# Optimization experiments

Hardware: AMD Instinct MI355X
Metric: run time of the kernel (lower is better)

The kernel has to match this reference:

```python
import jax, jax.numpy as jnp
import numpy as np

N_NODES, F_IN, HID, HEADS, REP, NCLS = 8192, 128, 64, 8, 512, 32
E, NSYN, LMAX = 2048, 4096, 8
DM, DI, DSTATE, DCONV, DTR = 512, 1024, 16, 4, 32


def setup_inputs():
    key = jax.random.key(0)
    ks = jax.random.split(key, 24)
    g = lambda i, shape, s=0.05: jax.random.normal(ks[i], shape, jnp.float32) * s
    return {
        "edge_attr": jax.random.normal(ks[0], (E, 8), jnp.float32),
        "synapse": jax.random.normal(ks[1], (NSYN, 6), jnp.float32),
        "x_param": g(2, (N_NODES, F_IN), 0.1),
        "W1": g(3, (F_IN, HEADS * HID)),
        "att_src1": g(4, (HEADS, HID), 0.1),
        "att_dst1": g(5, (HEADS, HID), 0.1),
        "b1": jnp.zeros((HEADS * HID,), jnp.float32),
        "W2": g(6, (HEADS * HID, REP)),
        "att_src2": g(7, (1, REP), 0.1),
        "att_dst2": g(8, (1, REP), 0.1),
        "b2": jnp.zeros((REP,), jnp.float32),
        "W_in": g(9, (6, DM), 0.1),
        "b_in": jnp.zeros((DM,), jnp.float32),
        "W_inproj": g(10, (DM, 2 * DI)),
        "conv_w": g(11, (DI, DCONV), 0.1),
        "conv_b": jnp.zeros((DI,), jnp.float32),
        "W_xproj": g(12, (DI, DTR + 2 * DSTATE)),
        "W_dt": g(13, (DTR, DI), 0.1),
        "b_dt": jnp.full((DI,), -4.0, jnp.float32),
        "A_log": jnp.log(jnp.tile(jnp.arange(1, DSTATE + 1, dtype=jnp.float32), (DI, 1))),
        "D": jnp.ones((DI,), jnp.float32),
        "W_outproj": g(14, (DI, DM)),
        "W_lout": g(15, (DM, DM)),
        "b_lout": jnp.zeros((DM,), jnp.float32),
        "Wc1": g(16, (REP + 2 * DM, 512)),
        "bc1": jnp.zeros((512,), jnp.float32),
        "Wc2": g(17, (512, NCLS)),
        "bc2": jnp.zeros((NCLS,), jnp.float32),
        "edge_index": jax.random.randint(ks[18], (2, E), 0, N_NODES),
        "synapse_index": jnp.sort(jax.random.randint(ks[19], (NSYN,), 0, E)),
        "scatter_size": N_NODES,
    }


def _gat(x, W, a_src, a_dst, bias, src, dst, heads, out_ch, concat):
    # PyG GATConv (eval mode, edge_dim=None, self-loops already appended to src/dst)
    n = x.shape[0]
    xw = (x @ W).reshape(n, heads, out_ch)
    e = (xw * a_src).sum(-1)[src] + (xw * a_dst).sum(-1)[dst]  # [E+N, H]
    e = jax.nn.leaky_relu(e, 0.2)
    m = jax.ops.segment_max(e, dst, num_segments=n)
    ex = jnp.exp(e - m[dst])
    denom = jax.ops.segment_sum(ex, dst, num_segments=n)
    alpha = ex / denom[dst]
    out = jax.ops.segment_sum(alpha[:, :, None] * xw[src], dst, num_segments=n)
    out = out.reshape(n, heads * out_ch) if concat else out.mean(1)
    return out + bias


def _mamba_encoder(synapse, synapse_index, W_in, b_in, W_inproj, conv_w, conv_b,
                   W_xproj, W_dt, b_dt, A_log, D, W_outproj, W_lout, b_lout):
    # ragged [NSYN,6] -> padded [E, LMAX, 6] (synapse_index is sorted)
    counts = jax.ops.segment_sum(jnp.ones((NSYN,), jnp.int32), synapse_index, num_segments=E)
    starts = jnp.cumsum(counts) - counts
    pos = jnp.arange(NSYN) - starts[synapse_index]
    padded = jnp.zeros((E, LMAX, synapse.shape[1]), synapse.dtype).at[
        synapse_index, pos].set(synapse, mode="drop")
    u = padded @ W_in + b_in                     # linear_in: [E, L, DM]
    xz = u @ W_inproj                            # in_proj:   [E, L, 2*DI]
    xm, z = xz[..., :DI], xz[..., DI:]
    # depthwise causal conv over time
    xc = jax.lax.conv_general_dilated(
        xm.transpose(0, 2, 1), conv_w[:, None, :],
        window_strides=(1,), padding=[(DCONV - 1, 0)],
        dimension_numbers=("NCH", "OIH", "NCH"), feature_group_count=DI)
    xc = jax.nn.silu(xc + conv_b[:, None]).transpose(0, 2, 1)  # [E, L, DI]
    xdb = xc @ W_xproj
    dt = jax.nn.softplus(xdb[..., :DTR] @ W_dt + b_dt)         # [E, L, DI]
    Bm = xdb[..., DTR:DTR + DSTATE]                            # [E, L, N]
    Cm = xdb[..., DTR + DSTATE:]                               # [E, L, N]
    A = -jnp.exp(A_log)                                        # [DI, N]

    def step(h, t):
        dt_t, B_t, C_t, x_t = t                                # [E,DI],[E,N],[E,N],[E,DI]
        h = jnp.exp(dt_t[:, :, None] * A) * h + (dt_t * x_t)[:, :, None] * B_t[:, None, :]
        return h, jnp.einsum("bdn,bn->bd", h, C_t)

    h0 = jnp.zeros((E, DI, DSTATE), xc.dtype)
    _, ys = jax.lax.scan(step, h0, (dt.transpose(1, 0, 2), Bm.transpose(1, 0, 2),
                                    Cm.transpose(1, 0, 2), xc.transpose(1, 0, 2)))
    y = ys.transpose(1, 0, 2) + D * xc                         # [E, L, DI]
    out = (y * jax.nn.silu(z)) @ W_outproj                     # [E, L, DM]
    # masked mean over true sequence length (empty groups behave like a zero seq of len 1)
    cnt = jnp.clip(counts, 1, LMAX).astype(out.dtype)
    mask = (jnp.arange(LMAX)[None, :] < cnt[:, None]).astype(out.dtype)
    pooled = (out * mask[:, :, None]).sum(1) / cnt[:, None]
    return pooled @ W_lout + b_lout                            # [E, DM]


def _forward(edge_attr, synapse, x_param, W1, att_src1, att_dst1, b1,
             W2, att_src2, att_dst2, b2, W_in, b_in, W_inproj, conv_w, conv_b,
             W_xproj, W_dt, b_dt, A_log, D, W_outproj, W_lout, b_lout,
             Wc1, bc1, Wc2, bc2, edge_index, synapse_index, scatter_size):
    # GAT stack (eval: dropouts identity; edge_attr unused since edge_dim=None)
    loops = jnp.arange(N_NODES)
    src = jnp.concatenate([edge_index[0], loops])
    dst = jnp.concatenate([edge_index[1], loops])
    h = jax.nn.elu(_gat(x_param, W1, att_src1, att_dst1, b1, src, dst, HEADS, HID, True))
    h = _gat(h, W2, att_src2, att_dst2, b2, src, dst, 1, REP, False)   # [N, REP]
    x_point = _mamba_encoder(synapse, synapse_index, W_in, b_in, W_inproj, conv_w,
                             conv_b, W_xproj, W_dt, b_dt, A_log, D, W_outproj,
                             W_lout, b_lout)                            # [E, DM]

    def smax(idx):
        s = jax.ops.segment_max(x_point, idx, num_segments=scatter_size)
        nz = jax.ops.segment_sum(jnp.ones((E,), jnp.int32), idx, num_segments=scatter_size)
        return jnp.where(nz[:, None] > 0, s, 0.0)  # torch_scatter: empty slots -> 0

    left, right = smax(edge_index[0]), smax(edge_index[1])
    feats = jnp.concatenate([h, left, right], axis=1)          # [N, REP+2*DM]
    return jax.nn.relu(feats @ Wc1 + bc1) @ Wc2 + bc2          # [N, NCLS]


def reference(edge_attr, synapse, x_param, W1, att_src1, att_dst1, b1,
              W2, att_src2, att_dst2, b2, W_in, b_in, W_inproj, conv_w, conv_b,
              W_xproj, W_dt, b_dt, A_log, D, W_outproj, W_lout, b_lout,
              Wc1, bc1, Wc2, bc2, edge_index, synapse_index, scatter_size):
    return _forward(edge_attr, synapse, x_param, W1, att_src1, att_dst1, b1,
                    W2, att_src2, att_dst2, b2, W_in, b_in, W_inproj, conv_w, conv_b,
                    W_xproj, W_dt, b_dt, A_log, D, W_outproj, W_lout, b_lout,
                    Wc1, bc1, Wc2, bc2, edge_index, synapse_index, scatter_size)
```

## Files before the change

kernel.cpp:

```cpp
#include <hip/hip_runtime.h>

#define N_NODES 8192
#define F_IN 128
#define HID 64
#define HEADS 8
#define REP 512
#define NCLS 32
#define E_EDGES 2048
#define NSYN 4096
#define LMAX 8
#define DM 512
#define DI 1024
#define DSTATE 16
#define DCONV 4
#define DTR 32
#define TOT_EDGES (E_EDGES + N_NODES)
#define ROWS (E_EDGES * LMAX)
#define MC_CAP 6144

typedef short bf16x8 __attribute__((ext_vector_type(8)));
typedef float f32x4 __attribute__((ext_vector_type(4)));

__device__ __forceinline__ unsigned mapf(float f) {
  unsigned u = __float_as_uint(f);
  return (u & 0x80000000u) ? ~u : (u | 0x80000000u);
}
__device__ __forceinline__ float unmapf(unsigned u) {
  return __uint_as_float((u & 0x80000000u) ? (u ^ 0x80000000u) : ~u);
}
__device__ __forceinline__ float fsig(float x) {
  return __builtin_amdgcn_rcpf(1.0f + __expf(-x));
}
__device__ __forceinline__ float fsoftplus(float x) {
  return fmaxf(x, 0.0f) + __logf(1.0f + __expf(-fabsf(x)));
}
__device__ __forceinline__ unsigned short f2bf(float f) {
  unsigned u = __float_as_uint(f);
  unsigned r = (u + 0x7FFFu + ((u >> 16) & 1u)) >> 16;
  return (unsigned short)r;
}
__device__ __forceinline__ float bf2f(unsigned short h) {
  return __uint_as_float(((unsigned)h) << 16);
}
__device__ __forceinline__ void split2(float x, unsigned short* hh, unsigned short* ll) {
  unsigned short h = f2bf(x);
  *hh = h;
  *ll = f2bf(x - bf2f(h));
}
__device__ __forceinline__ int lower_bound_dev(const int* __restrict__ arr, int n, int v) {
  int lo = 0, hi = n;
  while (lo < hi) { int mid = (lo + hi) >> 1; if (arr[mid] < v) lo = mid + 1; else hi = mid; }
  return lo;
}
__device__ __forceinline__ int src_of(const int* __restrict__ ei, int i) {
  return i < E_EDGES ? ei[i] : i - E_EDGES;
}
__device__ __forceinline__ int dst_of(const int* __restrict__ ei, int i) {
  return i < E_EDGES ? ei[E_EDGES + i] : i - E_EDGES;
}
__device__ __forceinline__ int clip_cnt(int c) { return c < 1 ? 1 : (c > LMAX ? LMAX : c); }

__global__ __launch_bounds__(256) void gemm_mfma(
    const unsigned short* __restrict__ Ah, const unsigned short* __restrict__ Al,
    const unsigned short* __restrict__ Bth, const unsigned short* __restrict__ Btl,
    float* __restrict__ C, int M, int N, int K,
    const float* __restrict__ bias, int act) {
  __shared__ __align__(16) unsigned short As[2][64][40];
  const int tid = threadIdx.x;
  const int w = tid >> 6;
  const int lane = tid & 63;
  const int brow = blockIdx.y * 64;
  const int bcol = blockIdx.x * 64;
  const int srow = tid >> 2;
  const int skc = tid & 3;
  const int r0 = lane & 15;
  const int kg = lane >> 4;
  f32x4 acc[4] = {};
  const size_t aoff = (size_t)(brow + srow) * K + skc * 8;
  const size_t boff = (size_t)(bcol + w * 16 + r0) * K + kg * 8;
  bf16x8 bh = *(const bf16x8*)(Bth + boff);
  bf16x8 bl = *(const bf16x8*)(Btl + boff);
  *(bf16x8*)(&As[0][srow][skc * 8]) = *(const bf16x8*)(Ah + aoff);
  *(bf16x8*)(&As[1][srow][skc * 8]) = *(const bf16x8*)(Al + aoff);
  __syncthreads();
  for (int kt = 0; kt < K; kt += 32) {
    const bool more = (kt + 32) < K;
    bf16x8 nAh, nAl, nbh, nbl;
    if (more) {
      nAh = *(const bf16x8*)(Ah + aoff + kt + 32);
      nAl = *(const bf16x8*)(Al + aoff + kt + 32);
      nbh = *(const bf16x8*)(Bth + boff + kt + 32);
      nbl = *(const bf16x8*)(Btl + boff + kt + 32);
    }
#pragma unroll
    for (int r = 0; r < 4; ++r) {
      bf16x8 ah = *(const bf16x8*)(&As[0][r * 16 + r0][kg * 8]);
      bf16x8 al = *(const bf16x8*)(&As[1][r * 16 + r0][kg * 8]);
      acc[r] = __builtin_amdgcn_mfma_f32_16x16x32_bf16(ah, bh, acc[r], 0, 0, 0);
      acc[r] = __builtin_amdgcn_mfma_f32_16x16x32_bf16(ah, bl, acc[r], 0, 0, 0);
      acc[r] = __builtin_amdgcn_mfma_f32_16x16x32_bf16(al, bh, acc[r], 0, 0, 0);
    }
    __syncthreads();
    if (more) {
      *(bf16x8*)(&As[0][srow][skc * 8]) = nAh;
      *(bf16x8*)(&As[1][srow][skc * 8]) = nAl;
      bh = nbh; bl = nbl;
    }
    __syncthreads();
  }
  const int col = bcol + w * 16 + r0;
  const float bb = bias ? bias[col] : 0.0f;
#pragma unroll
  for (int r = 0; r < 4; ++r) {
#pragma unroll
    for (int j = 0; j < 4; ++j) {
      int row = brow + r * 16 + kg * 4 + j;
      float v = acc[r][j] + bb;
      if (act == 1) v = fmaxf(v, 0.0f);
      C[(size_t)row * N + col] = v;
    }
  }
}

__global__ __launch_bounds__(512) void gemm_mfma2(
    const unsigned short* __restrict__ Ah, const unsigned short* __restrict__ Al,
    const unsigned short* __restrict__ Bth, const unsigned short* __restrict__ Btl,
    float* __restrict__ C, int M, int N, int K,
    const float* __restrict__ bias, int act) {
  __shared__ __align__(16) unsigned short As[2][128][40];
  __shared__ __align__(16) unsigned short Bs[2][128][40];
  const int tid = threadIdx.x;
  const int w = tid >> 6;
  const int lane = tid & 63;
  const int wr = w >> 2, wc = w & 3;
  const int mb = M >> 7;
  const int lin = blockIdx.x;
  const int bx = lin / mb;
  const int by = lin % mb;
  const int brow = by * 128;
  const int bcol = bx * 128;
  const int r0 = lane & 15;
  const int kg = lane >> 4;
  const int row0 = tid >> 2, kc0 = tid & 3;
  const size_t a0 = (size_t)(brow + row0) * K + kc0 * 8;
  const size_t b0 = (size_t)(bcol + row0) * K + kc0 * 8;
  f32x4 acc[4][2] = {};
  {
    bf16x8 t0 = *(const bf16x8*)(Ah + a0), t1 = *(const bf16x8*)(Al + a0);
    bf16x8 t2 = *(const bf16x8*)(Bth + b0), t3 = *(const bf16x8*)(Btl + b0);
    *(bf16x8*)(&As[0][row0][kc0 * 8]) = t0;
    *(bf16x8*)(&As[1][row0][kc0 * 8]) = t1;
    *(bf16x8*)(&Bs[0][row0][kc0 * 8]) = t2;
    *(bf16x8*)(&Bs[1][row0][kc0 * 8]) = t3;
  }
  __syncthreads();
  for (int kt = 0; kt < K; kt += 32) {
    const bool more = (kt + 32) < K;
    bf16x8 p0, p1, p2, p3;
    if (more) {
      p0 = *(const bf16x8*)(Ah + a0 + kt + 32);
      p1 = *(const bf16x8*)(Al + a0 + kt + 32);
      p2 = *(const bf16x8*)(Bth + b0 + kt + 32);
      p3 = *(const bf16x8*)(Btl + b0 + kt + 32);
    }
    bf16x8 bhv[2], blv[2];
#pragma unroll
    for (int cf = 0; cf < 2; ++cf) {
      bhv[cf] = *(const bf16x8*)(&Bs[0][wc * 32 + cf * 16 + r0][kg * 8]);
      blv[cf] = *(const bf16x8*)(&Bs[1][wc * 32 + cf * 16 + r0][kg * 8]);
    }
#pragma unroll
    for (int rf = 0; rf < 4; ++rf) {
      bf16x8 ah = *(const bf16x8*)(&As[0][wr * 64 + rf * 16 + r0][kg * 8]);
      bf16x8 al = *(const bf16x8*)(&As[1][wr * 64 + rf * 16 + r0][kg * 8]);
#pragma unroll
      for (int cf = 0; cf < 2; ++cf) {
        acc[rf][cf] = __builtin_amdgcn_mfma_f32_16x16x32_bf16(ah, bhv[cf], acc[rf][cf], 0, 0, 0);
        acc[rf][cf] = __builtin_amdgcn_mfma_f32_16x16x32_bf16(ah, blv[cf], acc[rf][cf], 0, 0, 0);
        acc[rf][cf] = __builtin_amdgcn_mfma_f32_16x16x32_bf16(al, bhv[cf], acc[rf][cf], 0, 0, 0);
      }
    }
    __syncthreads();
    if (more) {
      *(bf16x8*)(&As[0][row0][kc0 * 8]) = p0;
      *(bf16x8*)(&As[1][row0][kc0 * 8]) = p1;
      *(bf16x8*)(&Bs[0][row0][kc0 * 8]) = p2;
      *(bf16x8*)(&Bs[1][row0][kc0 * 8]) = p3;
    }
    __syncthreads();
  }
#pragma unroll
  for (int rf = 0; rf < 4; ++rf)
#pragma unroll
    for (int cf = 0; cf < 2; ++cf) {
      int col = bcol + wc * 32 + cf * 16 + r0;
      float bb = bias ? bias[col] : 0.0f;
#pragma unroll
      for (int j = 0; j < 4; ++j) {
        int row = brow + wr * 64 + rf * 16 + kg * 4 + j;
        float v = acc[rf][cf][j] + bb;
        if (act == 1) v = fmaxf(v, 0.0f);
        C[(size_t)row * N + col] = v;
      }
    }
}

__global__ __launch_bounds__(256) void gemm_mfma_sk(
    const unsigned short* __restrict__ Ah, const unsigned short* __restrict__ Al,
    const unsigned short* __restrict__ Bth, const unsigned short* __restrict__ Btl,
    float* __restrict__ C, int M, int N, int K) {
  __shared__ __align__(16) unsigned short As[2][64][40];
  const int tid = threadIdx.x;
  const int w = tid >> 6;
  const int lane = tid & 63;
  const int brow = blockIdx.y * 64;
  const int bcol = blockIdx.x * 64;
  const int srow = tid >> 2;
  const int skc = tid & 3;
  const int r0 = lane & 15;
  const int kg = lane >> 4;
  const int kchunk = K / gridDim.z;
  const int k0 = blockIdx.z * kchunk;
  f32x4 acc[4] = {};
  const size_t aoff = (size_t)(brow + srow) * K;
  const size_t boff = (size_t)(bcol + w * 16 + r0) * K + kg * 8;
  for (int kt = k0; kt < k0 + kchunk; kt += 32) {
    bf16x8 bh = *(const bf16x8*)(Bth + boff + kt);
    bf16x8 bl = *(const bf16x8*)(Btl + boff + kt);
    *(bf16x8*)(&As[0][srow][skc * 8]) = *(const bf16x8*)(Ah + aoff + kt + skc * 8);
    *(bf16x8*)(&As[1][srow][skc * 8]) = *(const bf16x8*)(Al + aoff + kt + skc * 8);
    __syncthreads();
#pragma unroll
    for (int r = 0; r < 4; ++r) {
      bf16x8 ah = *(const bf16x8*)(&As[0][r * 16 + r0][kg * 8]);
      bf16x8 al = *(const bf16x8*)(&As[1][r * 16 + r0][kg * 8]);
      acc[r] = __builtin_amdgcn_mfma_f32_16x16x32_bf16(ah, bh, acc[r], 0, 0, 0);
      acc[r] = __builtin_amdgcn_mfma_f32_16x16x32_bf16(ah, bl, acc[r], 0, 0, 0);
      acc[r] = __builtin_amdgcn_mfma_f32_16x16x32_bf16(al, bh, acc[r], 0, 0, 0);
    }
    __syncthreads();
  }
  const int col = bcol + w * 16 + r0;
#pragma unroll
  for (int r = 0; r < 4; ++r) {
#pragma unroll
    for (int j = 0; j < 4; ++j) {
      int row = brow + r * 16 + kg * 4 + j;
      atomicAdd(&C[(size_t)row * N + col], acc[r][j]);
    }
  }
}

__global__ void split_kernel(const float* __restrict__ x, unsigned short* __restrict__ h,
                             unsigned short* __restrict__ l, int n) {
  int i = blockIdx.x * 256 + threadIdx.x;
  if (i >= n) return;
  split2(x[i], &h[i], &l[i]);
}

__global__ void tsplit_kernel(const float* __restrict__ W, unsigned short* __restrict__ Wth,
                              unsigned short* __restrict__ Wtl, int K, int N) {
  int i = blockIdx.x * 256 + threadIdx.x;
  if (i >= K * N) return;
  int k = i / N, n = i - k * N;
  float v = W[i];
  unsigned short h = f2bf(v);
  Wth[(size_t)n * K + k] = h;
  Wtl[(size_t)n * K + k] = f2bf(v - bf2f(h));
}

template <int BM, int BN>
__global__ __launch_bounds__(256) void gemm_t(
    const float* __restrict__ A, int lda,
    const float* __restrict__ B, int ldb,
    float* __restrict__ C, int ldc,
    int M, int N, int K,
    const float* __restrict__ bias, int act) {
  constexpr int RR = BM / 64;
  constexpr int CR = BN / 64;
  __shared__ float As[16][BM + 4];
  __shared__ float Bs[16][BN + 4];
  const int tid = threadIdx.x;
  const int tx = tid & 15;
  const int ty = tid >> 4;
  const int brow = blockIdx.y * BM;
  const int bcol = blockIdx.x * BN;
  float acc[RR][CR][4][4] = {};
  for (int kt = 0; kt < K; kt += 16) {
#pragma unroll
    for (int p = 0; p < RR; ++p) {
      int c = tid + p * 256;
      int row = c >> 2, kc = c & 3;
      int gr = brow + row;
      float4 v = make_float4(0.f, 0.f, 0.f, 0.f);
      if (gr < M) v = *reinterpret_cast<const float4*>(A + (size_t)gr * lda + kt + kc * 4);
      As[kc * 4 + 0][row] = v.x;
      As[kc * 4 + 1][row] = v.y;
      As[kc * 4 + 2][row] = v.z;
      As[kc * 4 + 3][row] = v.w;
    }
#pragma unroll
    for (int p = 0; p < CR; ++p) {
      int c = tid + p * 256;
      int k = c / (BN / 4), c4 = c % (BN / 4);
      int gc = bcol + c4 * 4;
      float4 v = make_float4(0.f, 0.f, 0.f, 0.f);
      if (gc < N) v = *reinterpret_cast<const float4*>(B + (size_t)(kt + k) * ldb + gc);
      *reinterpret_cast<float4*>(&Bs[k][c4 * 4]) = v;
    }
    __syncthreads();
#pragma unroll
    for (int k = 0; k < 16; ++k) {
      float av[RR * 4], bv[CR * 4];
#pragma unroll
      for (int r = 0; r < RR; ++r) {
        float4 t = *reinterpret_cast<const float4*>(&As[k][r * 64 + ty * 4]);
        av[r * 4 + 0] = t.x; av[r * 4 + 1] = t.y; av[r * 4 + 2] = t.z; av[r * 4 + 3] = t.w;
      }
#pragma unroll
      for (int cq = 0; cq < CR; ++cq) {
        float4 t = *reinterpret_cast<const float4*>(&Bs[k][cq * 64 + tx * 4]);
        bv[cq * 4 + 0] = t.x; bv[cq * 4 + 1] = t.y; bv[cq * 4 + 2] = t.z; bv[cq * 4 + 3] = t.w;
      }
#pragma unroll
      for (int r = 0; r < RR; ++r)
#pragma unroll
        for (int cq = 0; cq < CR; ++cq)
#pragma unroll
          for (int i = 0; i < 4; ++i)
#pragma unroll
            for (int j = 0; j < 4; ++j)
              acc[r][cq][i][j] = fmaf(av[r * 4 + i], bv[cq * 4 + j], acc[r][cq][i][j]);
    }
    __syncthreads();
  }
#pragma unroll
  for (int r = 0; r < RR; ++r)
#pragma unroll
    for (int i = 0; i < 4; ++i) {
      int row = brow + r * 64 + ty * 4 + i;
      if (row >= M) continue;
#pragma unroll
      for (int cq = 0; cq < CR; ++cq) {
        int col = bcol + cq * 64 + tx * 4;
        if (col >= N) continue;
        float4 v;
        v.x = acc[r][cq][i][0]; v.y = acc[r][cq][i][1];
        v.z = acc[r][cq][i][2]; v.w = acc[r][cq][i][3];
        if (bias) {
          float4 bb = *reinterpret_cast<const float4*>(bias + col);
          v.x += bb.x; v.y += bb.y; v.z += bb.z; v.w += bb.w;
        }
        if (act == 1) {
          v.x = fmaxf(v.x, 0.f); v.y = fmaxf(v.y, 0.f);
          v.z = fmaxf(v.z, 0.f); v.w = fmaxf(v.w, 0.f);
        }
        *reinterpret_cast<float4*>(C + (size_t)row * ldc + col) = v;
      }
    }
}

__global__ void counts_kernel(const int* __restrict__ sidx, int* __restrict__ counts) {
  int e = blockIdx.x * 256 + threadIdx.x;
  if (e >= E_EDGES) return;
  int lo = lower_bound_dev(sidx, NSYN, e);
  int hi = lower_bound_dev(sidx, NSYN, e + 1);
  counts[e] = hi - lo;
}

__global__ void scatter_padded_kernel(const float* __restrict__ synapse,
                                      const int* __restrict__ sidx,
                                      float* __restrict__ padded) {
  int i = blockIdx.x * 256 + threadIdx.x;
  if (i >= NSYN) return;
  int e = sidx[i];
  int lo = lower_bound_dev(sidx, NSYN, e);
  int pos = i - lo;
  if (pos < LMAX) {
#pragma unroll
    for (int c = 0; c < 6; ++c) padded[((size_t)e * LMAX + pos) * 6 + c] = synapse[(size_t)i * 6 + c];
  }
}

__global__ __launch_bounds__(256) void prefix_kernel(const int* __restrict__ counts,
                                                     int* __restrict__ starts_c) {
  __shared__ int part[256];
  int t = threadIdx.x;
  int loc[8];
  int s = 0;
#pragma unroll
  for (int i = 0; i < 8; ++i) {
    int c = clip_cnt(counts[t * 8 + i]);
    loc[i] = s;
    s += c;
  }
  part[t] = s;
  __syncthreads();
  int mytot = s;
  for (int o = 1; o < 256; o <<= 1) {
    int add = (t >= o) ? part[t - o] : 0;
    __syncthreads();
    part[t] += add;
    __syncthreads();
  }
  int off = part[t] - mytot;
#pragma unroll
  for (int i = 0; i < 8; ++i) starts_c[t * 8 + i] = off + loc[i];
}

__global__ __launch_bounds__(256) void xc_compact_kernel(
    const float* __restrict__ padded,
    const float* __restrict__ W_eff, const float* __restrict__ b_eff,
    const float* __restrict__ conv_w, const float* __restrict__ conv_b,
    const int* __restrict__ counts, const int* __restrict__ starts_c,
    unsigned short* __restrict__ xch, unsigned short* __restrict__ xcl) {
  __shared__ float pads[LMAX * 6];
  int t = threadIdx.x;
  int d = blockIdx.x * 256 + t;
  int e = blockIdx.y;
  if (t < LMAX * 6) pads[t] = padded[(size_t)e * LMAX * 6 + t];
  __syncthreads();
  int cnt = clip_cnt(counts[e]);
  int sc = starts_c[e];
  float wef[6];
#pragma unroll
  for (int c = 0; c < 6; ++c) wef[c] = W_eff[c * 2048 + d];
  float cw0 = conv_w[d * 4 + 0], cw1 = conv_w[d * 4 + 1];
  float cw2 = conv_w[d * 4 + 2], cw3 = conv_w[d * 4 + 3];
  float cb = conv_b[d], be = b_eff[d];
  float x0 = 0.f, x1 = 0.f, x2 = 0.f;
  for (int l = 0; l < cnt; ++l) {
    float xm = be;
#pragma unroll
    for (int c = 0; c < 6; ++c) xm += pads[l * 6 + c] * wef[c];
    float s0 = cb + xm * cw3;
    if (l >= 1) s0 += x2 * cw2;
    if (l >= 2) s0 += x1 * cw1;
    if (l >= 3) s0 += x0 * cw0;
    float v = s0 * fsig(s0);
    size_t o = (size_t)(sc + l) * DI + d;
    split2(v, &xch[o], &xcl[o]);
    x0 = x1; x1 = x2; x2 = xm;
  }
}

__global__ __launch_bounds__(256) void mamba_scan_pool_kernel(
    const float* __restrict__ xdb_c, const float* __restrict__ padded,
    const float* __restrict__ W_eff, const float* __restrict__ b_eff,
    const float* __restrict__ W_dt, const float* __restrict__ b_dt,
    const float* __restrict__ A_log, const float* __restrict__ Dv,
    const float* __restrict__ conv_w, const float* __restrict__ conv_b,
    const int* __restrict__ counts, const int* __restrict__ starts_c,
    unsigned short* __restrict__ pooledh, unsigned short* __restrict__ pooledl) {
  __shared__ float pads[LMAX * 6];
  int t = threadIdx.x;
  int d = blockIdx.x * 256 + t;
  int e = blockIdx.y;
  if (t < LMAX * 6) pads[t] = padded[(size_t)e * LMAX * 6 + t];
  float wdt[DTR];
#pragma unroll
  for (int k = 0; k < DTR; ++k) wdt[k] = W_dt[k * DI + d];
  float a[DSTATE];
#pragma unroll
  for (int n = 0; n < DSTATE; ++n) a[n] = -__expf(A_log[d * DSTATE + n]);
  float h[DSTATE];
#pragma unroll
  for (int n = 0; n < DSTATE; ++n) h[n] = 0.0f;
  float wef[6], wez[6];
#pragma unroll
  for (int c = 0; c < 6; ++c) {
    wef[c] = W_eff[c * 2048 + d];
    wez[c] = W_eff[c * 2048 + DI + d];
  }
  float cw0 = conv_w[d * 4 + 0], cw1 = conv_w[d * 4 + 1];
  float cw2 = conv_w[d * 4 + 2], cw3 = conv_w[d * 4 + 3];
  float cb = conv_b[d];
  float bdt = b_dt[d], Dd = Dv[d], be = b_eff[d], bez = b_eff[DI + d];
  __syncthreads();
  int cnt = clip_cnt(counts[e]);
  int sc = starts_c[e];
  float x0 = 0.f, x1 = 0.f, x2 = 0.f;
  float ssum = 0.0f;
  for (int l = 0; l < cnt; ++l) {
    float xm = be;
#pragma unroll
    for (int c = 0; c < 6; ++c) xm += pads[l * 6 + c] * wef[c];
    float s0 = cb + xm * cw3;
    if (l >= 1) s0 += x2 * cw2;
    if (l >= 2) s0 += x1 * cw1;
    if (l >= 3) s0 += x0 * cw0;
    float xt = s0 * fsig(s0);
    const float* __restrict__ xrow = xdb_c + (size_t)(sc + l) * 64;
    float acc = bdt;
#pragma unroll
    for (int k = 0; k < DTR; ++k) acc += xrow[k] * wdt[k];
    float dt = fsoftplus(acc);
    float dtx = dt * xt;
    float y = 0.0f;
#pragma unroll
    for (int n = 0; n < DSTATE; ++n) {
      float en = __expf(dt * a[n]);
      h[n] = en * h[n] + dtx * xrow[32 + n];
      y += h[n] * xrow[48 + n];
    }
    y += Dd * xt;
    float z = bez;
#pragma unroll
    for (int c = 0; c < 6; ++c) z += pads[l * 6 + c] * wez[c];
    ssum += y * z * fsig(z);
    x0 = x1; x1 = x2; x2 = xm;
  }
  float pv = ssum / (float)cnt;
  split2(pv, &pooledh[(size_t)e * DI + d], &pooledl[(size_t)e * DI + d]);
}

__global__ void esed1_kernel(const float* __restrict__ xw1, const float* __restrict__ as1,
                             const float* __restrict__ ad1, float* __restrict__ es1,
                             float* __restrict__ ed1) {
  int idx = blockIdx.x * 256 + threadIdx.x;
  int n = idx >> 3, h = idx & 7;
  const float* xr = xw1 + (size_t)n * 512 + h * 64;
  const float* sr = as1 + h * 64;
  const float* dr = ad1 + h * 64;
  float es = 0.0f, ed = 0.0f;
#pragma unroll
  for (int c = 0; c < 64; ++c) { float v = xr[c]; es += v * sr[c]; ed += v * dr[c]; }
  es1[idx] = es; ed1[idx] = ed;
}

__global__ void edge1_kernel(const int* __restrict__ ei, const float* __restrict__ es1,
                             const float* __restrict__ ed1, float* __restrict__ e1,
                             unsigned* __restrict__ m1u) {
  int idx = blockIdx.x * 256 + threadIdx.x;
  if (idx >= TOT_EDGES * HEADS) return;
  int i = idx >> 3, h = idx & 7;
  int s = src_of(ei, i), d = dst_of(ei, i);
  float v = es1[s * 8 + h] + ed1[d * 8 + h];
  v = v >= 0.0f ? v : 0.2f * v;
  e1[idx] = v;
  atomicMax(m1u + d * 8 + h, mapf(v));
}

__global__ void ex1_kernel(const int* __restrict__ ei, float* __restrict__ e1,
                           const unsigned* __restrict__ m1u, float* __restrict__ denom1) {
  int idx = blockIdx.x * 256 + threadIdx.x;
  if (idx >= TOT_EDGES * HEADS) return;
  int i = idx >> 3, h = idx & 7;
  int d = dst_of(ei, i);
  float ex = expf(e1[idx] - unmapf(m1u[d * 8 + h]));
  e1[idx] = ex;
  atomicAdd(denom1 + d * 8 + h, ex);
}

__global__ void selfinit1_kernel(const float* __restrict__ e1, const float* __restrict__ denom1,
                                 const float* __restrict__ xw1, float* __restrict__ g1) {
  int idx = blockIdx.x * 256 + threadIdx.x;
  int n = idx >> 9, j = idx & 511;
  int h = j >> 6;
  float alpha = e1[(size_t)(E_EDGES + n) * 8 + h] / denom1[n * 8 + h];
  g1[idx] = alpha * xw1[idx];
}

__global__ __launch_bounds__(256) void agg1_kernel(const int* __restrict__ ei,
                                                   const float* __restrict__ e1,
                                                   const float* __restrict__ denom1,
                                                   const float* __restrict__ xw1,
                                                   float* __restrict__ g1) {
  int i = blockIdx.x;
  int s = ei[i], d = ei[E_EDGES + i];
  for (int j = threadIdx.x; j < 512; j += 256) {
    int h = j >> 6;
    float alpha = e1[i * 8 + h] / denom1[d * 8 + h];
    atomicAdd(g1 + (size_t)d * 512 + j, alpha * xw1[(size_t)s * 512 + j]);
  }
}

__global__ void elu_bias_split_kernel(const float* __restrict__ g1, const float* __restrict__ b1,
                                      unsigned short* __restrict__ g1h,
                                      unsigned short* __restrict__ g1l) {
  int idx = blockIdx.x * 256 + threadIdx.x;
  int j = idx & 511;
  float v = g1[idx] + b1[j];
  v = v > 0.0f ? v : expm1f(v);
  split2(v, &g1h[idx], &g1l[idx]);
}

__global__ __launch_bounds__(64) void esed2_kernel(const float* __restrict__ xw2,
                                                   const float* __restrict__ as2,
                                                   const float* __restrict__ ad2,
                                                   float* __restrict__ es2,
                                                   float* __restrict__ ed2) {
  int n = blockIdx.x, t = threadIdx.x;
  float es = 0.0f, ed = 0.0f;
  for (int c = t; c < 512; c += 64) {
    float v = xw2[(size_t)n * 512 + c];
    es += v * as2[c]; ed += v * ad2[c];
  }
#pragma unroll
  for (int o = 32; o > 0; o >>= 1) { es += __shfl_down(es, o, 64); ed += __shfl_down(ed, o, 64); }
  if (t == 0) { es2[n] = es; ed2[n] = ed; }
}

__global__ void edge2_kernel(const int* __restrict__ ei, const float* __restrict__ es2,
                             const float* __restrict__ ed2, float* __restrict__ e2,
                             unsigned* __restrict__ m2u) {
  int i = blockIdx.x * 256 + threadIdx.x;
  if (i >= TOT_EDGES) return;
  int s = src_of(ei, i), d = dst_of(ei, i);
  float v = es2[s] + ed2[d];
  v = v >= 0.0f ? v : 0.2f * v;
  e2[i] = v;
  atomicMax(m2u + d, mapf(v));
}

__global__ void ex2_kernel(const int* __restrict__ ei, float* __restrict__ e2,
                           const unsigned* __restrict__ m2u, float* __restrict__ denom2) {
  int i = blockIdx.x * 256 + threadIdx.x;
  if (i >= TOT_EDGES) return;
  int d = dst_of(ei, i);
  float ex = expf(e2[i] - unmapf(m2u[d]));
  e2[i] = ex;
  atomicAdd(denom2 + d, ex);
}

__global__ void selfinit2_kernel(const float* __restrict__ e2, const float* __restrict__ denom2,
                                 const float* __restrict__ xw2, float* __restrict__ g2) {
  int idx = blockIdx.x * 256 + threadIdx.x;
  int n = idx >> 9;
  float alpha = e2[E_EDGES + n] / denom2[n];
  g2[idx] = alpha * xw2[idx];
}

__global__ __launch_bounds__(256) void agg2_kernel(const int* __restrict__ ei,
                                                   const float* __restrict__ e2,
                                                   const float* __restrict__ denom2,
                                                   const float* __restrict__ xw2,
                                                   float* __restrict__ g2) {
  int i = blockIdx.x;
  int s = ei[i], d = ei[E_EDGES + i];
  float alpha = e2[i] / denom2[d];
  for (int j = threadIdx.x; j < 512; j += 256) {
    atomicAdd(g2 + (size_t)d * 512 + j, alpha * xw2[(size_t)s * 512 + j]);
  }
}

__global__ __launch_bounds__(256) void leftright_kernel(const int* __restrict__ ei,
                                                        const float* __restrict__ xp,
                                                        unsigned* __restrict__ leftU,
                                                        unsigned* __restrict__ rightU,
                                                        int* __restrict__ flagL,
                                                        int* __restrict__ flagR) {
  int i = blockIdx.x;
  int s = ei[i], d = ei[E_EDGES + i];
  if (threadIdx.x == 0) { flagL[s] = 1; flagR[d] = 1; }
  for (int j = threadIdx.x; j < 512; j += 256) {
    unsigned v = mapf(xp[(size_t)i * 512 + j]);
    atomicMax(leftU + (size_t)s * 512 + j, v);
    atomicMax(rightU + (size_t)d * 512 + j, v);
  }
}

__global__ void concat_split_kernel(const float* __restrict__ g2, const float* __restrict__ b2,
                                    const unsigned* __restrict__ leftU,
                                    const unsigned* __restrict__ rightU,
                                    const int* __restrict__ flagL, const int* __restrict__ flagR,
                                    unsigned short* __restrict__ fh,
                                    unsigned short* __restrict__ fl) {
  int idx = blockIdx.x * 256 + threadIdx.x;
  int n = idx >> 9, j = idx & 511;
  size_t base = (size_t)n * 1536 + j;
  split2(g2[idx] + b2[j], &fh[base], &fl[base]);
  split2(flagL[n] ? unmapf(leftU[idx]) : 0.0f, &fh[base + 512], &fl[base + 512]);
  split2(flagR[n] ? unmapf(rightU[idx]) : 0.0f, &fh[base + 1024], &fl[base + 1024]);
}

extern "C" void kernel_launch(void* const* d_in, const int* in_sizes, int n_in,
                              void* d_out, int out_size, void* d_ws, size_t ws_size,
                              hipStream_t stream) {
  const float* synapse = (const float*)d_in[1];
  const float* x_param = (const float*)d_in[2];
  const float* W1 = (const float*)d_in[3];
  const float* as1 = (const float*)d_in[4];
  const float* ad1 = (const float*)d_in[5];
  const float* b1 = (const float*)d_in[6];
  const float* W2 = (const float*)d_in[7];
  const float* as2 = (const float*)d_in[8];
  const float* ad2 = (const float*)d_in[9];
  const float* b2 = (const float*)d_in[10];
  const float* W_in = (const float*)d_in[11];
  const float* b_in = (const float*)d_in[12];
  const float* W_inproj = (const float*)d_in[13];
  const float* conv_w = (const float*)d_in[14];
  const float* conv_b = (const float*)d_in[15];
  const float* W_xproj = (const float*)d_in[16];
  const float* W_dt = (const float*)d_in[17];
  const float* b_dt = (const float*)d_in[18];
  const float* A_log = (const float*)d_in[19];
  const float* Dv = (const float*)d_in[20];
  const float* W_outproj = (const float*)d_in[21];
  const float* W_lout = (const float*)d_in[22];
  const float* b_lout = (const float*)d_in[23];
  const float* Wc1 = (const float*)d_in[24];
  const float* bc1 = (const float*)d_in[25];
  const float* Wc2 = (const float*)d_in[26];
  const float* bc2 = (const float*)d_in[27];
  const int* edge_index = (const int*)d_in[28];
  const int* sidx = (const int*)d_in[29];
  float* out = (float*)d_out;

  const size_t MB = (size_t)1 << 20;
  const size_t KB = (size_t)1 << 10;
  char* ws = (char*)d_ws;
  unsigned short* xc_ch = (unsigned short*)(ws + 0);
  unsigned short* xc_cl = (unsigned short*)(ws + 16 * MB);
  float* xw1 = (float*)(ws + 0);
  float* g1 = (float*)(ws + 16 * MB);
  unsigned short* g1h = (unsigned short*)(ws + 32 * MB);
  unsigned short* g1l = (unsigned short*)(ws + 40 * MB);
  unsigned short* xph = (unsigned short*)(ws + 48 * MB);
  unsigned short* xpl = (unsigned short*)(ws + 50 * MB);
  unsigned short* W1th = (unsigned short*)(ws + 52 * MB);
  unsigned short* W1tl = (unsigned short*)(ws + 52 * MB + 128 * KB);
  float* xw2 = (float*)(ws + 48 * MB);
  unsigned short* W2th = (unsigned short*)(ws + 0);
  unsigned short* W2tl = (unsigned short*)(ws + 512 * KB);
  float* g2 = (float*)(ws + 0);
  unsigned short* featsh = (unsigned short*)(ws + 16 * MB);
  unsigned short* featsl = (unsigned short*)(ws + 40 * MB);
  float* hidden = (float*)(ws + 0);
  float* xdb_c = (float*)(ws + 64 * MB);
  unsigned short* pooledh = (unsigned short*)(ws + 68 * MB);
  unsigned short* pooledl = (unsigned short*)(ws + 72 * MB);
  unsigned short* Wxth = (unsigned short*)(ws + 76 * MB);
  unsigned short* Wxtl = (unsigned short*)(ws + 76 * MB + 128 * KB);
  float* Wmix = (float*)(ws + 77 * MB);
  unsigned short* Wmixth = (unsigned short*)(ws + 80 * MB);
  unsigned short* Wmixtl = (unsigned short*)(ws + 81 * MB);
  unsigned* leftU = (unsigned*)(ws + 64 * MB);
  unsigned* rightU = (unsigned*)(ws + 80 * MB);
  float* x_point = (float*)(ws + 96 * MB);
  unsigned short* Wc1th = (unsigned short*)(ws + 96 * MB);
  unsigned short* Wc1tl = (unsigned short*)(ws + 96 * MB + 1536 * KB);
  char* sm = ws + 100 * MB;
  float* es1 = (float*)(sm + 0);
  float* ed1 = (float*)(sm + 256 * KB);
  float* e1 = (float*)(sm + 512 * KB);
  unsigned* m1u = (unsigned*)(sm + 832 * KB);
  float* denom1 = (float*)(sm + 1088 * KB);
  float* es2 = (float*)(sm + 1344 * KB);
  float* ed2 = (float*)(sm + 1376 * KB);
  float* e2 = (float*)(sm + 1408 * KB);
  unsigned* m2u = (unsigned*)(sm + 1448 * KB);
  float* denom2 = (float*)(sm + 1480 * KB);
  int* flagL = (int*)(sm + 1512 * KB);
  int* flagR = (int*)(sm + 1544 * KB);
  float* padded = (float*)(ws + 106 * MB);
  int* counts = (int*)(ws + 106 * MB + 384 * KB);
  float* W_eff = (float*)(ws + 106 * MB + 400 * KB);
  float* b_eff = (float*)(ws + 106 * MB + 448 * KB);
  int* starts_c = (int*)(ws + 106 * MB + 456 * KB);

  auto g64 = [&](const float* A, int lda, const float* B, int ldb, float* C, int ldc,
                 int M, int N, int K, const float* bias, int act) {
    dim3 grid((N + 63) / 64, (M + 63) / 64);
    gemm_t<64, 64><<<grid, 256, 0, stream>>>(A, lda, B, ldb, C, ldc, M, N, K, bias, act);
  };
  auto gm = [&](const unsigned short* Ah, const unsigned short* Al,
                const unsigned short* Bth, const unsigned short* Btl, float* C,
                int M, int N, int K, const float* bias, int act) {
    dim3 grid(N / 64, M / 64);
    gemm_mfma<<<grid, 256, 0, stream>>>(Ah, Al, Bth, Btl, C, M, N, K, bias, act);
  };
  auto gm2 = [&](const unsigned short* Ah, const unsigned short* Al,
                 const unsigned short* Bth, const unsigned short* Btl, float* C,
                 int M, int N, int K, const float* bias, int act) {
    gemm_mfma2<<<(N / 128) * (M / 128), 512, 0, stream>>>(Ah, Al, Bth, Btl, C, M, N, K, bias,
                                                          act);
  };
  auto tsplit = [&](const float* W, unsigned short* th, unsigned short* tl, int K, int N) {
    tsplit_kernel<<<(K * N + 255) / 256, 256, 0, stream>>>(W, th, tl, K, N);
  };

  g64(W_in, DM, W_inproj, 2 * DI, W_eff, 2 * DI, 6, 2 * DI, DM, nullptr, 0);
  g64(b_in, DM, W_inproj, 2 * DI, b_eff, 2 * DI, 1, 2 * DI, DM, nullptr, 0);
  g64(W_outproj, DM, W_lout, DM, Wmix, DM, DI, DM, DM, nullptr, 0);

  hipMemsetAsync(padded, 0, (size_t)ROWS * 6 * 4, stream);
  scatter_padded_kernel<<<(NSYN + 255) / 256, 256, 0, stream>>>(synapse, sidx, padded);
  counts_kernel<<<(E_EDGES + 255) / 256, 256, 0, stream>>>(sidx, counts);
  prefix_kernel<<<1, 256, 0, stream>>>(counts, starts_c);
  xc_compact_kernel<<<dim3(DI / 256, E_EDGES), 256, 0, stream>>>(
      padded, W_eff, b_eff, conv_w, conv_b, counts, starts_c, xc_ch, xc_cl);
  tsplit(W_xproj, Wxth, Wxtl, DI, 64);
  hipMemsetAsync(xdb_c, 0, (size_t)MC_CAP * 64 * 4, stream);
  gemm_mfma_sk<<<dim3(1, MC_CAP / 64, 8), 256, 0, stream>>>(xc_ch, xc_cl, Wxth, Wxtl, xdb_c,
                                                            MC_CAP, 64, DI);
  mamba_scan_pool_kernel<<<dim3(DI / 256, E_EDGES), 256, 0, stream>>>(
      xdb_c, padded, W_eff, b_eff, W_dt, b_dt, A_log, Dv, conv_w, conv_b, counts, starts_c,
      pooledh, pooledl);
  tsplit(Wmix, Wmixth, Wmixtl, DI, DM);
  gm(pooledh, pooledl, Wmixth, Wmixtl, x_point, E_EDGES, DM, DI, b_lout, 0);

  split_kernel<<<(N_NODES * F_IN + 255) / 256, 256, 0, stream>>>(x_param, xph, xpl,
                                                                 N_NODES * F_IN);
  tsplit(W1, W1th, W1tl, F_IN, HEADS * HID);
  gm2(xph, xpl, W1th, W1tl, xw1, N_NODES, HEADS * HID, F_IN, nullptr, 0);
  esed1_kernel<<<(N_NODES * HEADS) / 256, 256, 0, stream>>>(xw1, as1, ad1, es1, ed1);
  hipMemsetAsync(m1u, 0, 512 * KB, stream);
  edge1_kernel<<<(TOT_EDGES * HEADS + 255) / 256, 256, 0, stream>>>(edge_index, es1, ed1, e1, m1u);
  ex1_kernel<<<(TOT_EDGES * HEADS + 255) / 256, 256, 0, stream>>>(edge_index, e1, m1u, denom1);
  selfinit1_kernel<<<(N_NODES * 512) / 256, 256, 0, stream>>>(e1, denom1, xw1, g1);
  agg1_kernel<<<E_EDGES, 256, 0, stream>>>(edge_index, e1, denom1, xw1, g1);
  elu_bias_split_kernel<<<(N_NODES * 512) / 256, 256, 0, stream>>>(g1, b1, g1h, g1l);

  tsplit(W2, W2th, W2tl, HEADS * HID, REP);
  gm2(g1h, g1l, W2th, W2tl, xw2, N_NODES, REP, HEADS * HID, nullptr, 0);
  esed2_kernel<<<N_NODES, 64, 0, stream>>>(xw2, as2, ad2, es2, ed2);
  hipMemsetAsync(m2u, 0, 128 * KB, stream);
  edge2_kernel<<<(TOT_EDGES + 255) / 256, 256, 0, stream>>>(edge_index, es2, ed2, e2, m2u);
  ex2_kernel<<<(TOT_EDGES + 255) / 256, 256, 0, stream>>>(edge_index, e2, m2u, denom2);
  selfinit2_kernel<<<(N_NODES * 512) / 256, 256, 0, stream>>>(e2, denom2, xw2, g2);
  agg2_kernel<<<E_EDGES, 256, 0, stream>>>(edge_index, e2, denom2, xw2, g2);

  hipMemsetAsync(leftU, 0, 32 * MB, stream);
  leftright_kernel<<<E_EDGES, 256, 0, stream>>>(edge_index, x_point, leftU, rightU, flagL, flagR);

  concat_split_kernel<<<(N_NODES * 512) / 256, 256, 0, stream>>>(g2, b2, leftU, rightU, flagL,
                                                                 flagR, featsh, featsl);
  tsplit(Wc1, Wc1th, Wc1tl, REP + 2 * DM, 512);
  gm2(featsh, featsl, Wc1th, Wc1tl, hidden, N_NODES, 512, REP + 2 * DM, bc1, 1);
  g64(hidden, 512, Wc2, NCLS, out, NCLS, N_NODES, NCLS, 512, bc2, 0);
}
```

Measured before the change: 454.5 us.

## Fuse fp32 split, ELU+bias, and concat into the big GEMM A-loaders

```diff
diff --git a/kernel.cpp b/kernel.cpp
--- a/kernel.cpp
+++ b/kernel.cpp
@@ -65,7 +65,7 @@
     const unsigned short* __restrict__ Bth, const unsigned short* __restrict__ Btl,
     float* __restrict__ C, int M, int N, int K,
     const float* __restrict__ bias, int act) {
-  __shared__ __align__(16) unsigned short As[2][64][40];
+  __shared__ __align__(16) unsigned short As[2][64][44];
   const int tid = threadIdx.x;
   const int w = tid >> 6;
   const int lane = tid & 63;
@@ -122,13 +122,71 @@
   }
 }
 
-__global__ __launch_bounds__(512) void gemm_mfma2(
-    const unsigned short* __restrict__ Ah, const unsigned short* __restrict__ Al,
+template <int MODE>
+__device__ __forceinline__ void loadA_f(
+    const float* __restrict__ A32, const float* __restrict__ addv,
+    const float* __restrict__ leftF, const float* __restrict__ rightF,
+    int grow, int k, int K, float4& f0, float4& f1, float4& a0, float4& a1) {
+  if constexpr (MODE == 0) {
+    const float* p = A32 + (size_t)grow * K + k;
+    f0 = *(const float4*)p; f1 = *(const float4*)(p + 4);
+  } else if constexpr (MODE == 1) {
+    const float* p = A32 + (size_t)grow * 512 + k;
+    f0 = *(const float4*)p; f1 = *(const float4*)(p + 4);
+    a0 = *(const float4*)(addv + k); a1 = *(const float4*)(addv + k + 4);
+  } else {
+    int sec = k >> 9, cc = k & 511;
+    const float* p = (sec == 0) ? A32 + (size_t)grow * 512 + cc
+                                : ((sec == 1) ? leftF : rightF) + (size_t)grow * 512 + cc;
+    f0 = *(const float4*)p; f1 = *(const float4*)(p + 4);
+    if (sec == 0) { a0 = *(const float4*)(addv + cc); a1 = *(const float4*)(addv + cc + 4); }
+  }
+}
+
+template <int MODE>
+__device__ __forceinline__ void stageA_f(
+    unsigned short* dstH, unsigned short* dstL, int k, int fL, int fR,
+    float4 f0, float4 f1, float4 a0, float4 a1) {
+  float v[8] = {f0.x, f0.y, f0.z, f0.w, f1.x, f1.y, f1.z, f1.w};
+  float av[8] = {a0.x, a0.y, a0.z, a0.w, a1.x, a1.y, a1.z, a1.w};
+  if constexpr (MODE == 1) {
+#pragma unroll
+    for (int j = 0; j < 8; ++j) {
+      float t = v[j] + av[j];
+      v[j] = t > 0.0f ? t : expm1f(t);
+    }
+  } else if constexpr (MODE == 2) {
+    int sec = k >> 9;
+    if (sec == 0) {
+#pragma unroll
+      for (int j = 0; j < 8; ++j) v[j] += av[j];
+    } else {
+      int fg = (sec == 1) ? fL : fR;
+#pragma unroll
+      for (int j = 0; j < 8; ++j) v[j] = fg ? unmapf(__float_as_uint(v[j])) : 0.0f;
+    }
+  }
+  bf16x8 H, L;
+#pragma unroll
+  for (int j = 0; j < 8; ++j) {
+    unsigned short hh, ll;
+    split2(v[j], &hh, &ll);
+    H[j] = (short)hh; L[j] = (short)ll;
+  }
+  *(bf16x8*)dstH = H;
+  *(bf16x8*)dstL = L;
+}
+
+template <int MODE>
+__global__ __launch_bounds__(512) void gemm_mfma2f(
+    const float* __restrict__ A32, const float* __restrict__ addv,
+    const float* __restrict__ leftF, const float* __restrict__ rightF,
+    const int* __restrict__ flagL, const int* __restrict__ flagR,
     const unsigned short* __restrict__ Bth, const unsigned short* __restrict__ Btl,
     float* __restrict__ C, int M, int N, int K,
     const float* __restrict__ bias, int act) {
-  __shared__ __align__(16) unsigned short As[2][128][40];
-  __shared__ __align__(16) unsigned short Bs[2][128][40];
+  __shared__ __align__(16) unsigned short As[2][128][44];
+  __shared__ __align__(16) unsigned short Bs[2][128][44];
   const int tid = threadIdx.x;
   const int w = tid >> 6;
   const int lane = tid & 63;
@@ -142,24 +200,26 @@
   const int r0 = lane & 15;
   const int kg = lane >> 4;
   const int row0 = tid >> 2, kc0 = tid & 3;
-  const size_t a0 = (size_t)(brow + row0) * K + kc0 * 8;
+  const int grow = brow + row0;
+  int fL = 0, fR = 0;
+  if constexpr (MODE == 2) { fL = flagL[grow]; fR = flagR[grow]; }
   const size_t b0 = (size_t)(bcol + row0) * K + kc0 * 8;
   f32x4 acc[4][2] = {};
   {
-    bf16x8 t0 = *(const bf16x8*)(Ah + a0), t1 = *(const bf16x8*)(Al + a0);
+    float4 f0{}, f1{}, a0{}, a1{};
+    loadA_f<MODE>(A32, addv, leftF, rightF, grow, kc0 * 8, K, f0, f1, a0, a1);
     bf16x8 t2 = *(const bf16x8*)(Bth + b0), t3 = *(const bf16x8*)(Btl + b0);
-    *(bf16x8*)(&As[0][row0][kc0 * 8]) = t0;
-    *(bf16x8*)(&As[1][row0][kc0 * 8]) = t1;
+    stageA_f<MODE>(&As[0][row0][kc0 * 8], &As[1][row0][kc0 * 8], kc0 * 8, fL, fR, f0, f1, a0, a1);
     *(bf16x8*)(&Bs[0][row0][kc0 * 8]) = t2;
     *(bf16x8*)(&Bs[1][row0][kc0 * 8]) = t3;
   }
   __syncthreads();
   for (int kt = 0; kt < K; kt += 32) {
     const bool more = (kt + 32) < K;
-    bf16x8 p0, p1, p2, p3;
+    float4 f0{}, f1{}, a0{}, a1{};
+    bf16x8 p2, p3;
     if (more) {
-      p0 = *(const bf16x8*)(Ah + a0 + kt + 32);
-      p1 = *(const bf16x8*)(Al + a0 + kt + 32);
+      loadA_f<MODE>(A32, addv, leftF, rightF, grow, kt + 32 + kc0 * 8, K, f0, f1, a0, a1);
       p2 = *(const bf16x8*)(Bth + b0 + kt + 32);
       p3 = *(const bf16x8*)(Btl + b0 + kt + 32);
     }
@@ -182,8 +242,8 @@
     }
     __syncthreads();
     if (more) {
-      *(bf16x8*)(&As[0][row0][kc0 * 8]) = p0;
-      *(bf16x8*)(&As[1][row0][kc0 * 8]) = p1;
+      stageA_f<MODE>(&As[0][row0][kc0 * 8], &As[1][row0][kc0 * 8], kt + 32 + kc0 * 8, fL, fR,
+                     f0, f1, a0, a1);
       *(bf16x8*)(&Bs[0][row0][kc0 * 8]) = p2;
       *(bf16x8*)(&Bs[1][row0][kc0 * 8]) = p3;
     }
@@ -209,7 +269,7 @@
     const unsigned short* __restrict__ Ah, const unsigned short* __restrict__ Al,
     const unsigned short* __restrict__ Bth, const unsigned short* __restrict__ Btl,
     float* __restrict__ C, int M, int N, int K) {
-  __shared__ __align__(16) unsigned short As[2][64][40];
+  __shared__ __align__(16) unsigned short As[2][64][44];
   const int tid = threadIdx.x;
   const int w = tid >> 6;
   const int lane = tid & 63;
@@ -251,13 +311,6 @@
   }
 }
 
-__global__ void split_kernel(const float* __restrict__ x, unsigned short* __restrict__ h,
-                             unsigned short* __restrict__ l, int n) {
-  int i = blockIdx.x * 256 + threadIdx.x;
-  if (i >= n) return;
-  split2(x[i], &h[i], &l[i]);
-}
-
 __global__ void tsplit_kernel(const float* __restrict__ W, unsigned short* __restrict__ Wth,
                               unsigned short* __restrict__ Wtl, int K, int N) {
   int i = blockIdx.x * 256 + threadIdx.x;
@@ -575,16 +628,6 @@
   }
 }
 
-__global__ void elu_bias_split_kernel(const float* __restrict__ g1, const float* __restrict__ b1,
-                                      unsigned short* __restrict__ g1h,
-                                      unsigned short* __restrict__ g1l) {
-  int idx = blockIdx.x * 256 + threadIdx.x;
-  int j = idx & 511;
-  float v = g1[idx] + b1[j];
-  v = v > 0.0f ? v : expm1f(v);
-  split2(v, &g1h[idx], &g1l[idx]);
-}
-
 __global__ __launch_bounds__(64) void esed2_kernel(const float* __restrict__ xw2,
                                                    const float* __restrict__ as2,
                                                    const float* __restrict__ ad2,
@@ -658,20 +701,6 @@
     atomicMax(leftU + (size_t)s * 512 + j, v);
     atomicMax(rightU + (size_t)d * 512 + j, v);
   }
-}
-
-__global__ void concat_split_kernel(const float* __restrict__ g2, const float* __restrict__ b2,
-                                    const unsigned* __restrict__ leftU,
-                                    const unsigned* __restrict__ rightU,
-                                    const int* __restrict__ flagL, const int* __restrict__ flagR,
-                                    unsigned short* __restrict__ fh,
-                                    unsigned short* __restrict__ fl) {
-  int idx = blockIdx.x * 256 + threadIdx.x;
-  int n = idx >> 9, j = idx & 511;
-  size_t base = (size_t)n * 1536 + j;
-  split2(g2[idx] + b2[j], &fh[base], &fl[base]);
-  split2(flagL[n] ? unmapf(leftU[idx]) : 0.0f, &fh[base + 512], &fl[base + 512]);
-  split2(flagR[n] ? unmapf(rightU[idx]) : 0.0f, &fh[base + 1024], &fl[base + 1024]);
 }
 
 extern "C" void kernel_launch(void* const* d_in, const int* in_sizes, int n_in,
@@ -715,19 +744,13 @@
   unsigned short* xc_cl = (unsigned short*)(ws + 16 * MB);
   float* xw1 = (float*)(ws + 0);
   float* g1 = (float*)(ws + 16 * MB);
-  unsigned short* g1h = (unsigned short*)(ws + 32 * MB);
-  unsigned short* g1l = (unsigned short*)(ws + 40 * MB);
-  unsigned short* xph = (unsigned short*)(ws + 48 * MB);
-  unsigned short* xpl = (unsigned short*)(ws + 50 * MB);
   unsigned short* W1th = (unsigned short*)(ws + 52 * MB);
   unsigned short* W1tl = (unsigned short*)(ws + 52 * MB + 128 * KB);
   float* xw2 = (float*)(ws + 48 * MB);
   unsigned short* W2th = (unsigned short*)(ws + 0);
   unsigned short* W2tl = (unsigned short*)(ws + 512 * KB);
   float* g2 = (float*)(ws + 0);
-  unsigned short* featsh = (unsigned short*)(ws + 16 * MB);
-  unsigned short* featsl = (unsigned short*)(ws + 40 * MB);
-  float* hidden = (float*)(ws + 0);
+  float* hidden = (float*)(ws + 16 * MB);
   float* xdb_c = (float*)(ws + 64 * MB);
   unsigned short* pooledh = (unsigned short*)(ws + 68 * MB);
   unsigned short* pooledl = (unsigned short*)(ws + 72 * MB);
@@ -771,12 +794,6 @@
     dim3 grid(N / 64, M / 64);
     gemm_mfma<<<grid, 256, 0, stream>>>(Ah, Al, Bth, Btl, C, M, N, K, bias, act);
   };
-  auto gm2 = [&](const unsigned short* Ah, const unsigned short* Al,
-                 const unsigned short* Bth, const unsigned short* Btl, float* C,
-                 int M, int N, int K, const float* bias, int act) {
-    gemm_mfma2<<<(N / 128) * (M / 128), 512, 0, stream>>>(Ah, Al, Bth, Btl, C, M, N, K, bias,
-                                                          act);
-  };
   auto tsplit = [&](const float* W, unsigned short* th, unsigned short* tl, int K, int N) {
     tsplit_kernel<<<(K * N + 255) / 256, 256, 0, stream>>>(W, th, tl, K, N);
   };
@@ -801,20 +818,21 @@
   tsplit(Wmix, Wmixth, Wmixtl, DI, DM);
   gm(pooledh, pooledl, Wmixth, Wmixtl, x_point, E_EDGES, DM, DI, b_lout, 0);
 
-  split_kernel<<<(N_NODES * F_IN + 255) / 256, 256, 0, stream>>>(x_param, xph, xpl,
-                                                                 N_NODES * F_IN);
   tsplit(W1, W1th, W1tl, F_IN, HEADS * HID);
-  gm2(xph, xpl, W1th, W1tl, xw1, N_NODES, HEADS * HID, F_IN, nullptr, 0);
+  gemm_mfma2f<0><<<(512 / 128) * (N_NODES / 128), 512, 0, stream>>>(
+      x_param, nullptr, nullptr, nullptr, nullptr, nullptr, W1th, W1tl, xw1,
+      N_NODES, HEADS * HID, F_IN, nullptr, 0);
   esed1_kernel<<<(N_NODES * HEADS) / 256, 256, 0, stream>>>(xw1, as1, ad1, es1, ed1);
   hipMemsetAsync(m1u, 0, 512 * KB, stream);
   edge1_kernel<<<(TOT_EDGES * HEADS + 255) / 256, 256, 0, stream>>>(edge_index, es1, ed1, e1, m1u);
   ex1_kernel<<<(TOT_EDGES * HEADS + 255) / 256, 256, 0, stream>>>(edge_index, e1, m1u, denom1);
   selfinit1_kernel<<<(N_NODES * 512) / 256, 256, 0, stream>>>(e1, denom1, xw1, g1);
   agg1_kernel<<<E_EDGES, 256, 0, stream>>>(edge_index, e1, denom1, xw1, g1);
-  elu_bias_split_kernel<<<(N_NODES * 512) / 256, 256, 0, stream>>>(g1, b1, g1h, g1l);
 
   tsplit(W2, W2th, W2tl, HEADS * HID, REP);
-  gm2(g1h, g1l, W2th, W2tl, xw2, N_NODES, REP, HEADS * HID, nullptr, 0);
+  gemm_mfma2f<1><<<(REP / 128) * (N_NODES / 128), 512, 0, stream>>>(
+      g1, b1, nullptr, nullptr, nullptr, nullptr, W2th, W2tl, xw2,
+      N_NODES, REP, HEADS * HID, nullptr, 0);
   esed2_kernel<<<N_NODES, 64, 0, stream>>>(xw2, as2, ad2, es2, ed2);
   hipMemsetAsync(m2u, 0, 128 * KB, stream);
   edge2_kernel<<<(TOT_EDGES + 255) / 256, 256, 0, stream>>>(edge_index, es2, ed2, e2, m2u);
@@ -825,9 +843,9 @@
   hipMemsetAsync(leftU, 0, 32 * MB, stream);
   leftright_kernel<<<E_EDGES, 256, 0, stream>>>(edge_index, x_point, leftU, rightU, flagL, flagR);
 
-  concat_split_kernel<<<(N_NODES * 512) / 256, 256, 0, stream>>>(g2, b2, leftU, rightU, flagL,
-                                                                 flagR, featsh, featsl);
   tsplit(Wc1, Wc1th, Wc1tl, REP + 2 * DM, 512);
-  gm2(featsh, featsl, Wc1th, Wc1tl, hidden, N_NODES, 512, REP + 2 * DM, bc1, 1);
+  gemm_mfma2f<2><<<(512 / 128) * (N_NODES / 128), 512, 0, stream>>>(
+      g2, b2, (const float*)leftU, (const float*)rightU, flagL, flagR, Wc1th, Wc1tl, hidden,
+      N_NODES, 512, REP + 2 * DM, bc1, 1);
   g64(hidden, 512, Wc2, NCLS, out, NCLS, N_NODES, NCLS, 512, bc2, 0);
 }
```

Measured after the change: 481.1 us. 5.9% more time.
